# Kernel tuning notes

Measured on AMD Instinct MI355X. Metric: run time of the kernel, lower is better.

The kernel has to match this reference:

```python
import jax, jax.numpy as jnp
import numpy as np

B, L, D, Z, V, N, C = 4, 4096, 1024, 128, 1024, 16, 128
STD = 0.02
LN_EPS = 1e-5


def setup_inputs() -> dict:
    ks = jax.random.split(jax.random.key(0), 12)
    f32 = jnp.float32
    return {
        "x": jax.random.normal(ks[0], (B, L, D), dtype=f32),
        "ln1_g": jnp.ones((D,), f32), "ln1_b": jnp.zeros((D,), f32),
        "delta": jax.random.normal(ks[1], (D, N, 1), dtype=f32),
        "alpha": jax.random.normal(ks[2], (D, N, 1), dtype=f32),
        "beta_e": jax.random.normal(ks[3], (D, N, 1), dtype=f32) * STD,
        "gamma_e": jax.random.normal(ks[4], (D, N), dtype=f32),
        "omega": jax.random.normal(ks[5], (D,), dtype=f32) * STD,
        "Wv": jax.random.normal(ks[6], (D, V), dtype=f32) * STD, "bv": jnp.zeros((V,), f32),
        "Wmx": jax.random.normal(ks[7], (D, Z + V + 2 * D), dtype=f32) * STD, "bmx": jnp.zeros((Z + V + 2 * D,), f32),
        "Wh": jax.random.normal(ks[8], (V, D), dtype=f32) * STD, "bh": jnp.zeros((D,), f32),
        "gamma_g": jax.random.normal(ks[9], (2, Z), dtype=f32) * STD, "beta_g": jnp.zeros((2, Z), f32),
        "rpb": jax.random.normal(ks[10], (2 * C - 1,), dtype=f32) * STD,
        "ln2_g": jnp.ones((D,), f32), "ln2_b": jnp.zeros((D,), f32),
        "W1": jax.random.normal(ks[11], (D, 2 * D), dtype=f32) * STD, "b1": jnp.zeros((2 * D,), f32),
        "W2": jax.random.normal(jax.random.fold_in(ks[11], 1), (2 * D, D), dtype=f32) * STD, "b2": jnp.zeros((D,), f32),
    }


def layer_norm(x, g, b):
    m = jnp.mean(x, axis=-1, keepdims=True)
    xc = x - m
    v = jnp.mean(xc * xc, axis=-1, keepdims=True)
    return xc * jax.lax.rsqrt(v + LN_EPS) * g + b


def multi_head_ema(x, delta, alpha, beta_e, gamma_e, omega):
    # x: (B,L,D). Damped EMA SSM (MEGA), unidirectional, via causal FFT conv.
    p = jax.nn.sigmoid(delta)                      # (D,N,1)
    a = jax.nn.sigmoid(alpha)                      # (D,N,1)
    q = 1.0 - p * a                                # decay in (0,1)
    t = jnp.arange(L, dtype=x.dtype)               # (L,)
    vander = t[None, None, :] * jnp.log(q)         # (D,N,L)
    kern = (p * beta_e) * jnp.exp(vander)          # (D,N,L)
    scale = (1.0 / N) ** 0.5
    k = jnp.einsum('dnl,dn->dl', kern, gamma_e * scale)  # (D,L)
    n_fft = 2 * L
    xf = jnp.fft.rfft(x.transpose(0, 2, 1), n=n_fft)     # (B,D,F)
    kf = jnp.fft.rfft(k, n=n_fft)                        # (D,F)
    out = jnp.fft.irfft(xf * kf[None], n=n_fft)[..., :L] # (B,D,L) causal conv
    return out.transpose(0, 2, 1) + x * omega[None, None, :]


def simple_rel_pos_bias(rpb, c):
    # rpb: (2c-1,) -> (c,c) Toeplitz relative-position bias (MEGA 'simple')
    t = jnp.pad(rpb, (0, c))           # (3c-1,)
    t = jnp.tile(t, c)[:-c]            # (c*(3c-2),)
    t = t.reshape(c, 3 * c - 2)
    r = (2 * c - 1) // 2
    return t[:, r: t.shape[1] - r]     # (c,c)


def reference(x, ln1_g, ln1_b, delta, alpha, beta_e, gamma_e, omega, Wv, bv,
              Wmx, bmx, Wh, bh, gamma_g, beta_g, rpb, ln2_g, ln2_b, W1, b1, W2, b2):
    residual = x
    xn = layer_norm(x, ln1_g, ln1_b)                         # prenorm
    v = jax.nn.silu(xn @ Wv + bv)                            # (B,L,V)
    mx = jax.nn.silu(multi_head_ema(xn, delta, alpha, beta_e, gamma_e, omega))
    base = mx @ Wmx + bmx                                    # (B,L,D+Z+V+D)
    u = jax.nn.sigmoid(base[..., :D])                        # gate
    zr = jax.nn.silu(base[..., D:D + Z + V])
    hx = base[..., D + Z + V:]                               # (B,L,D)
    z, r = zr[..., :Z], zr[..., Z:]                          # (B,L,Z),(B,L,V)
    zz = z[..., None, :] * gamma_g + beta_g                  # (B,L,2,Z)
    q, k = zz[..., 0, :], zz[..., 1, :]
    K = L // C
    qc = q.reshape(B, K, C, Z) * (Z ** -0.5)
    kc = k.reshape(B, K, C, Z)
    vc = v.reshape(B, K, C, V)
    bias = simple_rel_pos_bias(rpb, C)                       # (C,C)
    scores = jnp.einsum('bkcz,bkdz->bkcd', qc, kc) + bias    # (B,K,C,C)
    attn = jax.nn.softmax(scores, axis=-1)
    h = jnp.einsum('bkcd,bkdv->bkcv', attn, vc).reshape(B, L, V)
    h = jax.nn.silu(hx + (h * r) @ Wh + bh)                  # (B,L,D)
    out = residual + u * (h - residual)                      # addcmul gate
    # FFN residual block (prenorm, residual 'R')
    y = layer_norm(out, ln2_g, ln2_b)
    y = jax.nn.silu(y @ W1 + b1) @ W2 + b2
    return out + y
```

## Files before the change

kernel.cpp:

```cpp
#include <hip/hip_runtime.h>
#include <hip/hip_bf16.h>

typedef __attribute__((ext_vector_type(8))) short bf16x8;
typedef __attribute__((ext_vector_type(4))) float f32x4;

#define DEV static __device__ __forceinline__

#define VMW(n) asm volatile("s_waitcnt vmcnt(" #n ")" ::: "memory")
#define BARX   asm volatile("s_barrier" ::: "memory")

DEV float bf2f(unsigned short u) {
    unsigned int x = ((unsigned int)u) << 16;
    return __builtin_bit_cast(float, x);
}
DEV unsigned short f2bf(float f) {
    unsigned int x = __builtin_bit_cast(unsigned int, f);
    unsigned int r = x + 0x7fffu + ((x >> 16) & 1u);
    return (unsigned short)(r >> 16);
}
DEV float sigmoidf_(float x) { return 1.f / (1.f + __expf(-x)); }
DEV float siluf_(float x)    { return x / (1.f + __expf(-x)); }

DEV void llds16(const unsigned short* g, unsigned short* l) {
    __builtin_amdgcn_global_load_lds((const __attribute__((address_space(1))) void*)g,
                                     (__attribute__((address_space(3))) void*)l, 16, 0, 0);
}

DEV void swz_xy(int& bx, int& by) {
    int gx = gridDim.x;
    int ychunk = gridDim.y >> 3;
    int n = blockIdx.y * gx + blockIdx.x;
    int idx = n >> 3;
    bx = idx / ychunk;
    by = (n & 7) * ychunk + (idx % ychunk);
}

DEV void mfma256(const unsigned short* __restrict__ A, const unsigned short* __restrict__ Bt,
                 int lda, int ldb, int KT, unsigned short* lds, f32x4 (&acc)[8][4])
{
    const int tid  = threadIdx.x;
    const int lane = tid & 63;
    const int w    = tid >> 6;
    const int wr   = (w >> 2) << 6;
    const int wc   = (w & 3) << 5;
    const int mr   = lane & 15;
    const int kq   = (lane >> 4) << 4;
    const int srow = tid >> 3;
    const int sw   = ((tid & 7) ^ (srow & 7)) << 3;

    const unsigned short* gA0 = A + (size_t)srow * lda + sw;
    const unsigned short* gA1 = gA0 + (size_t)128 * lda;
    const unsigned short* gB0 = Bt + (size_t)srow * ldb + sw;
    const unsigned short* gB1 = gB0 + (size_t)128 * ldb;
    const size_t a64 = (size_t)64 * lda, b64 = (size_t)64 * ldb;
    unsigned short* dst = lds + tid * 8;

    const int swz = (mr & 7) << 4;
    const int offK0 = kq ^ swz;
    const int offK1 = (64 + kq) ^ swz;
    const char* pAb = (const char*)lds + (wr + mr) * 128;
    const char* pBb = (const char*)lds + 32768 + (wc + mr) * 128;

#define STAGE8(NX) do { \
    unsigned short* d0 = dst + (NX) * 32768; \
    llds16(gA0, d0);          llds16(gA0 + a64, d0 + 4096);  gA0 += 64; \
    llds16(gB0, d0 + 16384);  llds16(gB0 + b64, d0 + 20480); gB0 += 64; \
    llds16(gB1, d0 + 24576);  llds16(gB1 + b64, d0 + 28672); gB1 += 64; \
    llds16(gA1, d0 + 8192);   llds16(gA1 + a64, d0 + 12288); gA1 += 64; \
} while (0)

    STAGE8(0);

    bf16x8 av[4][2], bA[2][2], bB[2][2];
    for (int kt = 0; kt < KT; ++kt) {
        VMW(0);
        BARX;
        if (kt + 1 < KT) STAGE8((kt & 1) ^ 1);
        const char* pA_ = pAb + (kt & 1) * 65536;
        const char* pB_ = pBb + (kt & 1) * 65536;
#pragma unroll
        for (int m = 0; m < 4; ++m) { av[m][0] = *(const bf16x8*)(pA_ + m * 2048 + offK0);
                                      av[m][1] = *(const bf16x8*)(pA_ + m * 2048 + offK1); }
#pragma unroll
        for (int n = 0; n < 2; ++n) { bA[n][0] = *(const bf16x8*)(pB_ + n * 2048 + offK0);
                                      bA[n][1] = *(const bf16x8*)(pB_ + n * 2048 + offK1); }
        __builtin_amdgcn_s_setprio(1);
#pragma unroll
        for (int m = 0; m < 4; ++m)
#pragma unroll
            for (int n = 0; n < 2; ++n) {
                acc[m][n] = __builtin_amdgcn_mfma_f32_16x16x32_bf16(av[m][0], bA[n][0], acc[m][n], 0, 0, 0);
                acc[m][n] = __builtin_amdgcn_mfma_f32_16x16x32_bf16(av[m][1], bA[n][1], acc[m][n], 0, 0, 0);
            }
        __builtin_amdgcn_s_setprio(0);
#pragma unroll
        for (int n = 0; n < 2; ++n) { bB[n][0] = *(const bf16x8*)(pB_ + 16384 + n * 2048 + offK0);
                                      bB[n][1] = *(const bf16x8*)(pB_ + 16384 + n * 2048 + offK1); }
        __builtin_amdgcn_s_setprio(1);
#pragma unroll
        for (int m = 0; m < 4; ++m)
#pragma unroll
            for (int n = 0; n < 2; ++n) {
                acc[m][2 + n] = __builtin_amdgcn_mfma_f32_16x16x32_bf16(av[m][0], bB[n][0], acc[m][2 + n], 0, 0, 0);
                acc[m][2 + n] = __builtin_amdgcn_mfma_f32_16x16x32_bf16(av[m][1], bB[n][1], acc[m][2 + n], 0, 0, 0);
            }
        __builtin_amdgcn_s_setprio(0);
#pragma unroll
        for (int m = 0; m < 4; ++m) { av[m][0] = *(const bf16x8*)(pA_ + 16384 + m * 2048 + offK0);
                                      av[m][1] = *(const bf16x8*)(pA_ + 16384 + m * 2048 + offK1); }
        __builtin_amdgcn_s_setprio(1);
#pragma unroll
        for (int m = 0; m < 4; ++m)
#pragma unroll
            for (int n = 0; n < 2; ++n) {
                acc[4 + m][n] = __builtin_amdgcn_mfma_f32_16x16x32_bf16(av[m][0], bA[n][0], acc[4 + m][n], 0, 0, 0);
                acc[4 + m][n] = __builtin_amdgcn_mfma_f32_16x16x32_bf16(av[m][1], bA[n][1], acc[4 + m][n], 0, 0, 0);
            }
        __builtin_amdgcn_s_setprio(0);
        __builtin_amdgcn_s_setprio(1);
#pragma unroll
        for (int m = 0; m < 4; ++m)
#pragma unroll
            for (int n = 0; n < 2; ++n) {
                acc[4 + m][2 + n] = __builtin_amdgcn_mfma_f32_16x16x32_bf16(av[m][0], bB[n][0], acc[4 + m][2 + n], 0, 0, 0);
                acc[4 + m][2 + n] = __builtin_amdgcn_mfma_f32_16x16x32_bf16(av[m][1], bB[n][1], acc[4 + m][2 + n], 0, 0, 0);
            }
        __builtin_amdgcn_s_setprio(0);
    }
#undef STAGE8
    BARX;
}

template <class F>
DEV void stage_rm(unsigned short* lds, const f32x4 (&acc)[8][4], F f)
{
    const int lane = threadIdx.x & 63, w = threadIdx.x >> 6;
    const int wr = (w >> 2) << 6, wc = (w & 3) << 5;
    const int rsub = (lane >> 4) << 2, csub = lane & 15;
#pragma unroll
    for (int i = 0; i < 8; ++i)
#pragma unroll
        for (int j = 0; j < 4; ++j) {
            int rl = ((i >> 2) << 7) + wr + ((i & 3) << 4) + rsub;
            int cl = ((j >> 1) << 7) + wc + ((j & 1) << 4) + csub;
#pragma unroll
            for (int jj = 0; jj < 4; ++jj) {
                int r = rl + jj;
                *(unsigned short*)((char*)lds + r * 512 + ((cl * 2) ^ (((r >> 2) & 3) << 5))) =
                    f(acc[i][j][jj], cl);
            }
        }
}
template <class F>
DEV void stage_cm(unsigned short* lds, const f32x4 (&acc)[8][4], F f)
{
    const int lane = threadIdx.x & 63, w = threadIdx.x >> 6;
    const int wr = (w >> 2) << 6, wc = (w & 3) << 5;
    const int rsub = (lane >> 4) << 2, csub = lane & 15;
#pragma unroll
    for (int i = 0; i < 8; ++i)
#pragma unroll
        for (int j = 0; j < 4; ++j) {
            int rl = ((i >> 2) << 7) + wr + ((i & 3) << 4) + rsub;
            int cl = ((j >> 1) << 7) + wc + ((j & 1) << 4) + csub;
            ushort4 p;
            p.x = f(acc[i][j][0], cl); p.y = f(acc[i][j][1], cl);
            p.z = f(acc[i][j][2], cl); p.w = f(acc[i][j][3], cl);
            *(ushort4*)((char*)lds + cl * 512 + ((rl * 2) ^ ((cl & 3) << 4))) = p;
        }
}
DEV bf16x8 rd_rm(const unsigned short* lds, int row, int cb) {
    return *(const bf16x8*)((const char*)lds + row * 512 + ((cb * 16) ^ (((row >> 2) & 3) << 5)));
}
DEV bf16x8 rd_cm(const unsigned short* lds, int col, int rb) {
    return *(const bf16x8*)((const char*)lds + col * 512 + ((rb * 16) ^ ((col & 3) << 4)));
}

DEV void mfma_loop(const unsigned short* __restrict__ A, const unsigned short* __restrict__ Bt,
                   int lda, int ldb, int K, unsigned short* lds, f32x4 acc[4][4])
{
    const int tid = threadIdx.x;
    const int lane = tid & 63;
    const int wid = tid >> 6;
    const int wm = wid >> 1, wn = wid & 1;
    const int row0 = tid >> 2,         cg0 = (tid & 3) * 8;
    const int row1 = (256 + tid) >> 2, cg1 = (tid & 3) * 8;
    const int dst0 = (tid - lane) * 8;
    const int dst1 = (256 + tid - lane) * 8;

    auto stage = [&](unsigned short* sbuf, int kt) {
        const unsigned short* gA = A + (size_t)kt * 32;
        const unsigned short* gB = Bt + (size_t)kt * 32;
        llds16(gA + (size_t)row0 * lda + cg0, sbuf + dst0);
        llds16(gA + (size_t)row1 * lda + cg1, sbuf + dst1);
        llds16(gB + (size_t)row0 * ldb + cg0, sbuf + 4096 + dst0);
        llds16(gB + (size_t)row1 * ldb + cg1, sbuf + 4096 + dst1);
    };

    const int KT = K >> 5;
    stage(lds, 0);
    __syncthreads();
    const int mr = lane & 15, kr = (lane >> 4) * 8;
    for (int kt = 0; kt < KT; ++kt) {
        unsigned short* sbuf = lds + (kt & 1) * 8192;
        if (kt + 1 < KT) stage(lds + ((kt + 1) & 1) * 8192, kt + 1);
        const unsigned short* sA = sbuf;
        const unsigned short* sB = sbuf + 4096;
        bf16x8 av[4], bv[4];
#pragma unroll
        for (int f = 0; f < 4; ++f) {
            av[f] = *(const bf16x8*)(sA + (wm * 64 + f * 16 + mr) * 32 + kr);
            bv[f] = *(const bf16x8*)(sB + (wn * 64 + f * 16 + mr) * 32 + kr);
        }
#pragma unroll
        for (int fm = 0; fm < 4; ++fm)
#pragma unroll
            for (int fn = 0; fn < 4; ++fn)
                acc[fm][fn] = __builtin_amdgcn_mfma_f32_16x16x32_bf16(av[fm], bv[fn], acc[fm][fn], 0, 0, 0);
        __syncthreads();
    }
}

__global__ void k_transpose(const float* __restrict__ W, unsigned short* __restrict__ Wt, int K, int N)
{
    __shared__ float tile[32][33];
    int n0 = blockIdx.x * 32, k0 = blockIdx.y * 32;
    for (int i = threadIdx.y; i < 32; i += 8)
        tile[i][threadIdx.x] = W[(size_t)(k0 + i) * N + n0 + threadIdx.x];
    __syncthreads();
    for (int i = threadIdx.y; i < 32; i += 8)
        Wt[(size_t)(n0 + i) * K + k0 + threadIdx.x] = f2bf(tile[threadIdx.x][i]);
}

__global__ __launch_bounds__(256) void k_ln(const float* __restrict__ x, const float* __restrict__ g,
                                            const float* __restrict__ b, unsigned short* __restrict__ o)
{
    size_t row = blockIdx.x;
    int tid = threadIdx.x;
    float4 v = ((const float4*)(x + row * 1024))[tid];
    float s = v.x + v.y + v.z + v.w;
    float sq = v.x * v.x + v.y * v.y + v.z * v.z + v.w * v.w;
#pragma unroll
    for (int off = 1; off < 64; off <<= 1) { s += __shfl_xor(s, off); sq += __shfl_xor(sq, off); }
    __shared__ float ls[4], lq[4];
    int wid = tid >> 6;
    if ((tid & 63) == 0) { ls[wid] = s; lq[wid] = sq; }
    __syncthreads();
    s = ls[0] + ls[1] + ls[2] + ls[3];
    sq = lq[0] + lq[1] + lq[2] + lq[3];
    float mean = s * (1.f / 1024.f);
    float var = sq * (1.f / 1024.f) - mean * mean;
    float rstd = rsqrtf(var + 1e-5f);
    float4 gv = ((const float4*)g)[tid];
    float4 bv = ((const float4*)b)[tid];
    ushort4 p;
    p.x = f2bf((v.x - mean) * rstd * gv.x + bv.x);
    p.y = f2bf((v.y - mean) * rstd * gv.y + bv.y);
    p.z = f2bf((v.z - mean) * rstd * gv.z + bv.z);
    p.w = f2bf((v.w - mean) * rstd * gv.w + bv.w);
    ((ushort4*)(o + row * 1024))[tid] = p;
}

#define SEG 128
#define NSEG 32

__global__ __launch_bounds__(64) void k_ema_a(const unsigned short* __restrict__ xn,
                                              const float* __restrict__ delta, const float* __restrict__ alpha,
                                              float* __restrict__ st)
{
    int d = blockIdx.x * 64 + threadIdx.x;
    int s = blockIdx.y, b = blockIdx.z;
    float q[16], h[16];
#pragma unroll
    for (int n = 0; n < 16; ++n) {
        float p = sigmoidf_(delta[d * 16 + n]);
        float a = sigmoidf_(alpha[d * 16 + n]);
        q[n] = 1.f - p * a; h[n] = 0.f;
    }
    const unsigned short* xp = xn + ((size_t)b * 4096 + (size_t)s * SEG) * 1024 + d;
    for (int l = 0; l < SEG; ++l) {
        float xv = bf2f(xp[(size_t)l * 1024]);
#pragma unroll
        for (int n = 0; n < 16; ++n) h[n] = q[n] * h[n] + xv;
    }
    float* sp = st + (size_t)(b * 1024 + d) * 16 * NSEG;
#pragma unroll
    for (int n = 0; n < 16; ++n) sp[n * NSEG + s] = h[n];
}

__global__ void k_ema_b(const float* __restrict__ delta, const float* __restrict__ alpha, float* __restrict__ st)
{
    int gid = blockIdx.x * 256 + threadIdx.x;
    int n = gid & 15, d = (gid >> 4) & 1023;
    float p = sigmoidf_(delta[d * 16 + n]);
    float a = sigmoidf_(alpha[d * 16 + n]);
    float qq = 1.f - p * a;
    float qs = qq;
#pragma unroll
    for (int i = 0; i < 7; ++i) qs *= qs;
    float* sp = st + (size_t)gid * NSEG;
    float A_ = 0.f;
#pragma unroll
    for (int s = 0; s < NSEG; ++s) { float t = sp[s]; sp[s] = A_; A_ = qs * A_ + t; }
}

__global__ __launch_bounds__(64) void k_ema_c(const unsigned short* __restrict__ xn,
                                              const float* __restrict__ delta, const float* __restrict__ alpha,
                                              const float* __restrict__ beta_e, const float* __restrict__ gamma_e,
                                              const float* __restrict__ omega, const float* __restrict__ st,
                                              unsigned short* __restrict__ mxb)
{
    int d = blockIdx.x * 64 + threadIdx.x;
    int s = blockIdx.y, b = blockIdx.z;
    float q[16], c[16], h[16];
    const float* sp = st + (size_t)(b * 1024 + d) * 16 * NSEG;
#pragma unroll
    for (int n = 0; n < 16; ++n) {
        float p = sigmoidf_(delta[d * 16 + n]);
        float a = sigmoidf_(alpha[d * 16 + n]);
        q[n] = 1.f - p * a;
        c[n] = p * beta_e[d * 16 + n] * gamma_e[d * 16 + n] * 0.25f;
        h[n] = sp[n * NSEG + s];
    }
    float om = omega[d];
    const unsigned short* xp = xn + ((size_t)b * 4096 + (size_t)s * SEG) * 1024 + d;
    unsigned short* op = mxb + ((size_t)b * 4096 + (size_t)s * SEG) * 1024 + d;
    for (int l = 0; l < SEG; ++l) {
        float xv = bf2f(xp[(size_t)l * 1024]);
        float o = xv * om;
#pragma unroll
        for (int n = 0; n < 16; ++n) { h[n] = q[n] * h[n] + xv; o += c[n] * h[n]; }
        op[(size_t)l * 1024] = f2bf(siluf_(o));
    }
}

__global__ __launch_bounds__(512, 2) void k_gemm_v2_v(const unsigned short* __restrict__ xn,
                                                      const unsigned short* __restrict__ WvT,
                                                      const float* __restrict__ bv, unsigned short* __restrict__ vt)
{
    __shared__ __align__(16) unsigned short lds[65536];
    int bx, by; swz_xy(bx, by);
    int n0 = bx * 256, m0 = by * 256;
    f32x4 acc[8][4] = {};
    mfma256(xn + (size_t)m0 * 1024, WvT + (size_t)n0 * 1024, 1024, 1024, 16, lds, acc);
    stage_cm(lds, acc, [&](float v, int cl) -> unsigned short {
        return f2bf(siluf_(v + bv[n0 + cl]));
    });
    __syncthreads();
    const int t = threadIdx.x;
#pragma unroll
    for (int it = 0; it < 16; ++it) {
        int col = it * 16 + (t >> 5);
        int rb = t & 31;
        bf16x8 vv = rd_cm(lds, col, rb);
        int grow = m0 + rb * 8;
        size_t off = ((size_t)(grow >> 7) * 1024 + (n0 + col)) * 128 + (grow & 127);
        *(bf16x8*)(vt + off) = vv;
    }
}

__global__ __launch_bounds__(512, 2) void k_gemm_v2_mx(const unsigned short* __restrict__ mx,
                                                       const unsigned short* __restrict__ WmxT,
                                                       const float* __restrict__ bmx,
                                                       const float* __restrict__ gamma_g, const float* __restrict__ beta_g,
                                                       unsigned short* __restrict__ ub, unsigned short* __restrict__ qb,
                                                       unsigned short* __restrict__ kb, unsigned short* __restrict__ rb,
                                                       unsigned short* __restrict__ hxb)
{
    __shared__ __align__(16) unsigned short lds[65536];
    int bx, by; swz_xy(bx, by);
    int n0 = bx * 256, m0 = by * 256;
    f32x4 acc[8][4] = {};
    mfma256(mx + (size_t)m0 * 1024, WmxT + (size_t)n0 * 1024, 1024, 1024, 16, lds, acc);
    stage_rm(lds, acc, [&](float v, int cl) -> unsigned short {
        int gc = n0 + cl;
        if (gc >= 3200) return 0;
        float val = v + bmx[gc];
        if (gc < 1024) return f2bf(sigmoidf_(val));
        if (gc < 2176) return f2bf(siluf_(val));
        return f2bf(val);
    });
    __syncthreads();
    const int t = threadIdx.x;
#pragma unroll
    for (int it = 0; it < 16; ++it) {
        int row = it * 16 + (t >> 5);
        int cb = t & 31;
        int gc = n0 + cb * 8;
        if (gc >= 3200) continue;
        bf16x8 vv = rd_rm(lds, row, cb);
        size_t grow = m0 + row;
        if (gc < 1024) {
            *(bf16x8*)(ub + grow * 1024 + gc) = vv;
        } else if (gc < 1152) {
            int zc = gc - 1024;
            bf16x8 qv, kv;
#pragma unroll
            for (int e = 0; e < 8; ++e) {
                float z = bf2f((unsigned short)vv[e]);
                qv[e] = (short)f2bf((z * gamma_g[zc + e] + beta_g[zc + e]) * 0.088388347648318447f);
                kv[e] = (short)f2bf(z * gamma_g[128 + zc + e] + beta_g[128 + zc + e]);
            }
            *(bf16x8*)(qb + grow * 128 + zc) = qv;
            *(bf16x8*)(kb + grow * 128 + zc) = kv;
        } else if (gc < 2176) {
            *(bf16x8*)(rb + grow * 1024 + (gc - 1152)) = vv;
        } else {
            *(bf16x8*)(hxb + grow * 1024 + (gc - 2176)) = vv;
        }
    }
}

__global__ __launch_bounds__(256) void k_attn(const unsigned short* __restrict__ qb,
                                              const unsigned short* __restrict__ kb,
                                              const float* __restrict__ rpb, unsigned short* __restrict__ attn)
{
    __shared__ __align__(16) union U { unsigned short stage[16384]; unsigned short sc[128 * 132]; } sh;
    int bc = blockIdx.x;
    size_t t0 = (size_t)bc * 128;
    f32x4 acc[4][4] = {};
    mfma_loop(qb + t0 * 128, kb + t0 * 128, 128, 128, 128, sh.stage, acc);
    int tid = threadIdx.x, lane = tid & 63, wid = tid >> 6, wm = wid >> 1, wn = wid & 1;
#pragma unroll
    for (int fm = 0; fm < 4; ++fm)
#pragma unroll
        for (int fn = 0; fn < 4; ++fn) {
            int r = wm * 64 + fm * 16 + ((lane >> 4) << 2);
            int c = wn * 64 + fn * 16 + (lane & 15);
#pragma unroll
            for (int j = 0; j < 4; ++j) sh.sc[(r + j) * 132 + c] = f2bf(acc[fm][fn][j]);
        }
    __syncthreads();
    int row = tid >> 1, half = tid & 1;
    const unsigned short* srow = sh.sc + row * 132 + half * 64;
    const float* bp = rpb + 127 - row + half * 64;
    float v[64];
    float mxv = -1e30f;
#pragma unroll
    for (int i = 0; i < 64; ++i) { float s = bf2f(srow[i]) + bp[i]; v[i] = s; mxv = fmaxf(mxv, s); }
    mxv = fmaxf(mxv, __shfl_xor(mxv, 1));
    float sum = 0.f;
#pragma unroll
    for (int i = 0; i < 64; ++i) { float e = __expf(v[i] - mxv); v[i] = e; sum += e; }
    sum += __shfl_xor(sum, 1);
    float inv = 1.f / sum;
    unsigned short* arow = attn + ((size_t)bc * 128 + row) * 128 + half * 64;
#pragma unroll
    for (int i = 0; i < 64; ++i) arow[i] = f2bf(v[i] * inv);
}

__global__ __launch_bounds__(256) void k_gemm_pv(const unsigned short* __restrict__ attn,
                                                 const unsigned short* __restrict__ vt,
                                                 unsigned short* __restrict__ rhr)
{
    __shared__ __align__(16) unsigned short lds[16384];
    int bc = blockIdx.z;
    int n0 = blockIdx.x * 128;
    f32x4 acc[4][4] = {};
    mfma_loop(attn + (size_t)bc * 16384, vt + (size_t)bc * 131072 + (size_t)n0 * 128, 128, 128, 128, lds, acc);
    int lane = threadIdx.x & 63, wid = threadIdx.x >> 6, wm = wid >> 1, wn = wid & 1;
#pragma unroll
    for (int fm = 0; fm < 4; ++fm)
#pragma unroll
        for (int fn = 0; fn < 4; ++fn) {
            int rowb = wm * 64 + fm * 16 + ((lane >> 4) << 2);
            int col = n0 + wn * 64 + fn * 16 + (lane & 15);
#pragma unroll
            for (int j = 0; j < 4; ++j) {
                size_t m = (size_t)bc * 128 + rowb + j;
                size_t off = m * 1024 + col;
                rhr[off] = f2bf(acc[fm][fn][j] * bf2f(rhr[off]));
            }
        }
}

__global__ __launch_bounds__(512, 2) void k_gemm_v2_out(const unsigned short* __restrict__ hr,
                                                        const unsigned short* __restrict__ WhT,
                                                        const float* __restrict__ bh,
                                                        const unsigned short* __restrict__ hxb,
                                                        const unsigned short* __restrict__ ub,
                                                        const float* __restrict__ x, float* __restrict__ outp)
{
    __shared__ __align__(16) unsigned short lds[65536];
    int bx, by; swz_xy(bx, by);
    int n0 = bx * 256, m0 = by * 256;
    f32x4 acc[8][4] = {};
    mfma256(hr + (size_t)m0 * 1024, WhT + (size_t)n0 * 1024, 1024, 1024, 16, lds, acc);
    const int lane = threadIdx.x & 63, w = threadIdx.x >> 6;
    const int wr = (w >> 2) << 6, wc = (w & 3) << 5;
    const int rsub = (lane >> 4) << 2, csub = lane & 15;
#pragma unroll
    for (int i = 0; i < 8; ++i)
#pragma unroll
        for (int j = 0; j < 4; ++j) {
            int rowb = m0 + ((i >> 2) << 7) + wr + ((i & 3) << 4) + rsub;
            int col = n0 + ((j >> 1) << 7) + wc + ((j & 1) << 4) + csub;
            float bias = bh[col];
#pragma unroll
            for (int jj = 0; jj < 4; ++jj) {
                size_t off = (size_t)(rowb + jj) * 1024 + col;
                float g = acc[i][j][jj] + bias + bf2f(hxb[off]);
                float h2 = siluf_(g);
                float xv = x[off];
                outp[off] = xv + bf2f(ub[off]) * (h2 - xv);
            }
        }
}

__global__ __launch_bounds__(512, 2) void k_ffn1_v2(const unsigned short* __restrict__ yn,
                                                    const unsigned short* __restrict__ W1T,
                                                    const float* __restrict__ b1, unsigned short* __restrict__ t1)
{
    __shared__ __align__(16) unsigned short lds[65536];
    int bx, by; swz_xy(bx, by);
    int n0 = bx * 256, m0 = by * 256;
    f32x4 acc[8][4] = {};
    mfma256(yn + (size_t)m0 * 1024, W1T + (size_t)n0 * 1024, 1024, 1024, 16, lds, acc);
    stage_rm(lds, acc, [&](float v, int cl) -> unsigned short {
        return f2bf(siluf_(v + b1[n0 + cl]));
    });
    __syncthreads();
    const int t = threadIdx.x;
#pragma unroll
    for (int it = 0; it < 16; ++it) {
        int row = it * 16 + (t >> 5);
        int cb = t & 31;
        bf16x8 vv = rd_rm(lds, row, cb);
        *(bf16x8*)(t1 + (size_t)(m0 + row) * 2048 + n0 + cb * 8) = vv;
    }
}

__global__ __launch_bounds__(512, 2) void k_ffn2_v2(const unsigned short* __restrict__ t1,
                                                    const unsigned short* __restrict__ W2T,
                                                    const float* __restrict__ b2, float* __restrict__ outp)
{
    __shared__ __align__(16) unsigned short lds[65536];
    int bx, by; swz_xy(bx, by);
    int n0 = bx * 256, m0 = by * 256;
    f32x4 acc[8][4] = {};
    mfma256(t1 + (size_t)m0 * 2048, W2T + (size_t)n0 * 2048, 2048, 2048, 32, lds, acc);
    const int lane = threadIdx.x & 63, w = threadIdx.x >> 6;
    const int wr = (w >> 2) << 6, wc = (w & 3) << 5;
    const int rsub = (lane >> 4) << 2, csub = lane & 15;
#pragma unroll
    for (int i = 0; i < 8; ++i)
#pragma unroll
        for (int j = 0; j < 4; ++j) {
            int rowb = m0 + ((i >> 2) << 7) + wr + ((i & 3) << 4) + rsub;
            int col = n0 + ((j >> 1) << 7) + wc + ((j & 1) << 4) + csub;
            float bias = b2[col];
#pragma unroll
            for (int jj = 0; jj < 4; ++jj) {
                size_t off = (size_t)(rowb + jj) * 1024 + col;
                outp[off] = outp[off] + acc[i][j][jj] + bias;
            }
        }
}

extern "C" void kernel_launch(void* const* d_in, const int* in_sizes, int n_in,
                              void* d_out, int out_size, void* d_ws, size_t ws_size,
                              hipStream_t stream)
{
    (void)in_sizes; (void)n_in; (void)out_size; (void)ws_size;
    const float* x      = (const float*)d_in[0];
    const float* ln1_g  = (const float*)d_in[1];
    const float* ln1_b  = (const float*)d_in[2];
    const float* delta  = (const float*)d_in[3];
    const float* alpha  = (const float*)d_in[4];
    const float* beta_e = (const float*)d_in[5];
    const float* gamma_e= (const float*)d_in[6];
    const float* omega  = (const float*)d_in[7];
    const float* Wv     = (const float*)d_in[8];
    const float* bv     = (const float*)d_in[9];
    const float* Wmx    = (const float*)d_in[10];
    const float* bmx    = (const float*)d_in[11];
    const float* Wh     = (const float*)d_in[12];
    const float* bh     = (const float*)d_in[13];
    const float* gamma_g= (const float*)d_in[14];
    const float* beta_g = (const float*)d_in[15];
    const float* rpb    = (const float*)d_in[16];
    const float* ln2_g  = (const float*)d_in[17];
    const float* ln2_b  = (const float*)d_in[18];
    const float* W1     = (const float*)d_in[19];
    const float* b1     = (const float*)d_in[20];
    const float* W2     = (const float*)d_in[21];
    const float* b2     = (const float*)d_in[22];
    float* outp = (float*)d_out;

    char* w = (char*)d_ws;
    unsigned short* xn   = (unsigned short*)(w + 0);
    unsigned short* at   = (unsigned short*)(w + 0);
    unsigned short* mxb  = (unsigned short*)(w + 33554432);
    unsigned short* t1   = (unsigned short*)(w + 0);
    unsigned short* vt   = (unsigned short*)(w + 67108864);
    unsigned short* ub   = (unsigned short*)(w + 100663296);
    unsigned short* hxb  = (unsigned short*)(w + 134217728);
    unsigned short* rb   = (unsigned short*)(w + 167772160);
    unsigned short* yn   = (unsigned short*)(w + 167772160);
    unsigned short* qb   = (unsigned short*)(w + 201326592);
    unsigned short* kb   = (unsigned short*)(w + 205520896);
    float*          st   = (float*)(w + 201326592);
    unsigned short* WvT  = (unsigned short*)(w + 209715200);
    unsigned short* WmxT = (unsigned short*)(w + 211812352);
    unsigned short* WhT  = (unsigned short*)(w + 218628096);
    unsigned short* W1T  = (unsigned short*)(w + 220725248);
    unsigned short* W2T  = (unsigned short*)(w + 224919552);

    dim3 tb(32, 8);
    k_transpose<<<dim3(32, 32), tb, 0, stream>>>(Wv, WvT, 1024, 1024);
    k_transpose<<<dim3(100, 32), tb, 0, stream>>>(Wmx, WmxT, 1024, 3200);
    k_transpose<<<dim3(32, 32), tb, 0, stream>>>(Wh, WhT, 1024, 1024);
    k_transpose<<<dim3(64, 32), tb, 0, stream>>>(W1, W1T, 1024, 2048);
    k_transpose<<<dim3(32, 64), tb, 0, stream>>>(W2, W2T, 2048, 1024);

    k_ln<<<16384, 256, 0, stream>>>(x, ln1_g, ln1_b, xn);

    k_ema_a<<<dim3(16, NSEG, 4), 64, 0, stream>>>(xn, delta, alpha, st);
    k_ema_b<<<256, 256, 0, stream>>>(delta, alpha, st);
    k_ema_c<<<dim3(16, NSEG, 4), 64, 0, stream>>>(xn, delta, alpha, beta_e, gamma_e, omega, st, mxb);

    k_gemm_v2_v<<<dim3(4, 64), 512, 0, stream>>>(xn, WvT, bv, vt);
    k_gemm_v2_mx<<<dim3(13, 64), 512, 0, stream>>>(mxb, WmxT, bmx, gamma_g, beta_g, ub, qb, kb, rb, hxb);
    k_attn<<<128, 256, 0, stream>>>(qb, kb, rpb, at);
    k_gemm_pv<<<dim3(8, 1, 128), 256, 0, stream>>>(at, vt, rb);
    k_gemm_v2_out<<<dim3(4, 64), 512, 0, stream>>>(rb, WhT, bh, hxb, ub, x, outp);
    k_ln<<<16384, 256, 0, stream>>>(outp, ln2_g, ln2_b, yn);
    k_ffn1_v2<<<dim3(8, 64), 512, 0, stream>>>(yn, W1T, b1, t1);
    k_ffn2_v2<<<dim3(4, 64), 512, 0, stream>>>(t1, W2T, b2, outp);
}
```

Measured before the change: 646.7 us.

## Interleave per-quarter global-to-LDS staging with MFMA phases in GEMM mainloop

Splits the next k-tile's global-to-LDS staging into four pieces (A0, B0, B1, A1) and issues each between the MFMA quarters, with partial vmcnt waits and extra barriers. The previous loop waited for every load and then staged the whole next tile at once. The goal is to spread memory traffic across the compute phases so the MFMA units see smaller bubbles at the top of each k-iteration. The cost is more s_barrier instructions per iteration, plus correctness that depends on the partial waits matching the staging order.

```diff
diff --git a/kernel.cpp b/kernel.cpp
--- a/kernel.cpp
+++ b/kernel.cpp
@@ -61,74 +61,81 @@
     const char* pAb = (const char*)lds + (wr + mr) * 128;
     const char* pBb = (const char*)lds + 32768 + (wc + mr) * 128;
 
-#define STAGE8(NX) do { \
-    unsigned short* d0 = dst + (NX) * 32768; \
-    llds16(gA0, d0);          llds16(gA0 + a64, d0 + 4096);  gA0 += 64; \
-    llds16(gB0, d0 + 16384);  llds16(gB0 + b64, d0 + 20480); gB0 += 64; \
-    llds16(gB1, d0 + 24576);  llds16(gB1 + b64, d0 + 28672); gB1 += 64; \
-    llds16(gA1, d0 + 8192);   llds16(gA1 + a64, d0 + 12288); gA1 += 64; \
+    auto stA0 = [&](int nx) { unsigned short* d0 = dst + nx * 32768;
+        llds16(gA0, d0);         llds16(gA0 + a64, d0 + 4096);  gA0 += 64; };
+    auto stB0 = [&](int nx) { unsigned short* d0 = dst + nx * 32768;
+        llds16(gB0, d0 + 16384); llds16(gB0 + b64, d0 + 20480); gB0 += 64; };
+    auto stB1 = [&](int nx) { unsigned short* d0 = dst + nx * 32768;
+        llds16(gB1, d0 + 24576); llds16(gB1 + b64, d0 + 28672); gB1 += 64; };
+    auto stA1 = [&](int nx) { unsigned short* d0 = dst + nx * 32768;
+        llds16(gA1, d0 + 8192);  llds16(gA1 + a64, d0 + 12288); gA1 += 64; };
+
+    stA0(0); stB0(0); stB1(0); stA1(0);
+    VMW(4);
+    BARX;
+
+    bf16x8 av[4][2], bA[2][2], bB[2][2];
+
+#define MFMA_Q(AOFF, BARR, NOFF) \
+    __builtin_amdgcn_s_setprio(1); \
+    _Pragma("unroll") \
+    for (int m = 0; m < 4; ++m) \
+        _Pragma("unroll") \
+        for (int n = 0; n < 2; ++n) { \
+            acc[AOFF + m][NOFF + n] = __builtin_amdgcn_mfma_f32_16x16x32_bf16(av[m][0], BARR[n][0], acc[AOFF + m][NOFF + n], 0, 0, 0); \
+            acc[AOFF + m][NOFF + n] = __builtin_amdgcn_mfma_f32_16x16x32_bf16(av[m][1], BARR[n][1], acc[AOFF + m][NOFF + n], 0, 0, 0); \
+        } \
+    __builtin_amdgcn_s_setprio(0)
+
+#define KTILE(W0, W1, W3, ST) do { \
+     \
+    _Pragma("unroll") \
+    for (int m = 0; m < 4; ++m) { av[m][0] = *(const bf16x8*)(pA_ + m * 2048 + offK0); \
+                                  av[m][1] = *(const bf16x8*)(pA_ + m * 2048 + offK1); } \
+    _Pragma("unroll") \
+    for (int n = 0; n < 2; ++n) { bA[n][0] = *(const bf16x8*)(pB_ + n * 2048 + offK0); \
+                                  bA[n][1] = *(const bf16x8*)(pB_ + n * 2048 + offK1); } \
+    if (ST) stA0(nx); \
+    VMW(W0); BARX; \
+    MFMA_Q(0, bA, 0); \
+    BARX; \
+     \
+    _Pragma("unroll") \
+    for (int n = 0; n < 2; ++n) { bB[n][0] = *(const bf16x8*)(pB_ + 16384 + n * 2048 + offK0); \
+                                  bB[n][1] = *(const bf16x8*)(pB_ + 16384 + n * 2048 + offK1); } \
+    if (ST) stB0(nx); \
+    VMW(W1); BARX; \
+    MFMA_Q(0, bB, 2); \
+    BARX; \
+     \
+    _Pragma("unroll") \
+    for (int m = 0; m < 4; ++m) { av[m][0] = *(const bf16x8*)(pA_ + 16384 + m * 2048 + offK0); \
+                                  av[m][1] = *(const bf16x8*)(pA_ + 16384 + m * 2048 + offK1); } \
+    if (ST) stB1(nx); \
+    BARX; \
+    MFMA_Q(4, bA, 0); \
+    BARX; \
+     \
+    if (ST) stA1(nx); \
+    VMW(W3); BARX; \
+    MFMA_Q(4, bB, 2); \
+    BARX; \
 } while (0)
 
-    STAGE8(0);
-
-    bf16x8 av[4][2], bA[2][2], bB[2][2];
-    for (int kt = 0; kt < KT; ++kt) {
-        VMW(0);
-        BARX;
-        if (kt + 1 < KT) STAGE8((kt & 1) ^ 1);
+    for (int kt = 0; kt < KT - 1; ++kt) {
         const char* pA_ = pAb + (kt & 1) * 65536;
         const char* pB_ = pBb + (kt & 1) * 65536;
-#pragma unroll
-        for (int m = 0; m < 4; ++m) { av[m][0] = *(const bf16x8*)(pA_ + m * 2048 + offK0);
-                                      av[m][1] = *(const bf16x8*)(pA_ + m * 2048 + offK1); }
-#pragma unroll
-        for (int n = 0; n < 2; ++n) { bA[n][0] = *(const bf16x8*)(pB_ + n * 2048 + offK0);
-                                      bA[n][1] = *(const bf16x8*)(pB_ + n * 2048 + offK1); }
-        __builtin_amdgcn_s_setprio(1);
-#pragma unroll
-        for (int m = 0; m < 4; ++m)
-#pragma unroll
-            for (int n = 0; n < 2; ++n) {
-                acc[m][n] = __builtin_amdgcn_mfma_f32_16x16x32_bf16(av[m][0], bA[n][0], acc[m][n], 0, 0, 0);
-                acc[m][n] = __builtin_amdgcn_mfma_f32_16x16x32_bf16(av[m][1], bA[n][1], acc[m][n], 0, 0, 0);
-            }
-        __builtin_amdgcn_s_setprio(0);
-#pragma unroll
-        for (int n = 0; n < 2; ++n) { bB[n][0] = *(const bf16x8*)(pB_ + 16384 + n * 2048 + offK0);
-                                      bB[n][1] = *(const bf16x8*)(pB_ + 16384 + n * 2048 + offK1); }
-        __builtin_amdgcn_s_setprio(1);
-#pragma unroll
-        for (int m = 0; m < 4; ++m)
-#pragma unroll
-            for (int n = 0; n < 2; ++n) {
-                acc[m][2 + n] = __builtin_amdgcn_mfma_f32_16x16x32_bf16(av[m][0], bB[n][0], acc[m][2 + n], 0, 0, 0);
-                acc[m][2 + n] = __builtin_amdgcn_mfma_f32_16x16x32_bf16(av[m][1], bB[n][1], acc[m][2 + n], 0, 0, 0);
-            }
-        __builtin_amdgcn_s_setprio(0);
-#pragma unroll
-        for (int m = 0; m < 4; ++m) { av[m][0] = *(const bf16x8*)(pA_ + 16384 + m * 2048 + offK0);
-                                      av[m][1] = *(const bf16x8*)(pA_ + 16384 + m * 2048 + offK1); }
-        __builtin_amdgcn_s_setprio(1);
-#pragma unroll
-        for (int m = 0; m < 4; ++m)
-#pragma unroll
-            for (int n = 0; n < 2; ++n) {
-                acc[4 + m][n] = __builtin_amdgcn_mfma_f32_16x16x32_bf16(av[m][0], bA[n][0], acc[4 + m][n], 0, 0, 0);
-                acc[4 + m][n] = __builtin_amdgcn_mfma_f32_16x16x32_bf16(av[m][1], bA[n][1], acc[4 + m][n], 0, 0, 0);
-            }
-        __builtin_amdgcn_s_setprio(0);
-        __builtin_amdgcn_s_setprio(1);
-#pragma unroll
-        for (int m = 0; m < 4; ++m)
-#pragma unroll
-            for (int n = 0; n < 2; ++n) {
-                acc[4 + m][2 + n] = __builtin_amdgcn_mfma_f32_16x16x32_bf16(av[m][0], bB[n][0], acc[4 + m][2 + n], 0, 0, 0);
-                acc[4 + m][2 + n] = __builtin_amdgcn_mfma_f32_16x16x32_bf16(av[m][1], bB[n][1], acc[4 + m][2 + n], 0, 0, 0);
-            }
-        __builtin_amdgcn_s_setprio(0);
-    }
-#undef STAGE8
-    BARX;
+        const int nx = (kt & 1) ^ 1;
+        KTILE(4, 4, 4, true);
+    }
+    {
+        const char* pA_ = pAb + ((KT - 1) & 1) * 65536;
+        const char* pB_ = pBb + ((KT - 1) & 1) * 65536;
+        const int nx = 0; (void)nx;
+        KTILE(2, 0, 0, false);
+    }
+#undef KTILE
+#undef MFMA_Q
 }
 
 template <class F>
```

New measurement: 653.2 us. No clear change (+1.0%).
